# Performance work log

Measured on AMD Instinct MI355X. Metric: run time of the kernel, lower is better.

## Reference

```python
import jax, jax.numpy as jnp
import numpy as np
from jax import lax

RESI_RATIO = 0.5  # abs(quant_resi=-0.5)
BETA = 0.25


def setup_inputs() -> dict:
    key = jax.random.key(0)
    k1, k2, k3, k4 = jax.random.split(key, 4)
    B, C, T, H, W = 2, 32, 8, 32, 32
    V = 8192
    f_BCTHW = jax.random.normal(k1, (B, C, T, H, W), dtype=jnp.float32)
    emb_weight = jax.random.normal(k2, (V, C), dtype=jnp.float32)
    conv_w = jax.random.normal(k3, (C, C, 3, 3, 3), dtype=jnp.float32) * 0.02
    conv_b = jax.random.normal(k4, (C,), dtype=jnp.float32) * 0.02
    return {"f_BCTHW": f_BCTHW, "emb_weight": emb_weight, "conv_w": conv_w, "conv_b": conv_b}


def _mse(a, b):
    d = a - b
    return jnp.mean(d * d)


def reference(f_BCTHW, emb_weight, conv_w, conv_b):
    f = f_BCTHW.astype(jnp.float32)
    B, C, T, H, W = f.shape
    V = emb_weight.shape[0]

    # ---- nearest-codebook assignment (vocab_norm=False path) ----
    # query uses detached f (stop_gradient) exactly as torch .detach()
    q = lax.stop_gradient(f).transpose(0, 2, 3, 4, 1).reshape(-1, C)  # [N, C]
    emb_sg = lax.stop_gradient(emb_weight)
    # ||q||^2 + ||e||^2 - 2 q.e  (addmm_ with alpha=-2, beta=1)
    dist = (jnp.sum(q * q, axis=1, keepdims=True)
            + jnp.sum(emb_sg * emb_sg, axis=1)
            - 2.0 * (q @ emb_sg.T))  # [N, V]
    idx_N = jnp.argmin(dist, axis=1)  # [N] int

    # ---- usage stats (bincount) ----
    counts = jnp.zeros((V,), jnp.float32).at[idx_N].add(1.0)
    prob = counts / jnp.sum(counts)
    vocab_usage = jnp.mean((prob > (0.01 / V)).astype(jnp.float32)) * 100.0

    # ---- embedding gather + residual conv blend ----
    fh = emb_weight[idx_N].reshape(B, T, H, W, C).transpose(0, 4, 1, 2, 3)  # [B,C,T,H,W]
    conv = lax.conv_general_dilated(
        fh, conv_w, window_strides=(1, 1, 1), padding='SAME',
        dimension_numbers=('NCDHW', 'OIDHW', 'NCDHW'))
    conv = conv + conv_b[None, :, None, None, None]
    fh = fh * (1.0 - RESI_RATIO) + conv * RESI_RATIO

    # ---- VQ loss + straight-through estimator ----
    vq_loss = BETA * _mse(lax.stop_gradient(fh), f) + _mse(fh, lax.stop_gradient(f))
    fhat = lax.stop_gradient(fh - f) + f

    return fhat, vq_loss, vocab_usage
```

## Files before the change

kernel.cpp:

```cpp
#include <hip/hip_runtime.h>

#define NQ    16384
#define CDIM  32
#define VSZ   8192
#define PLANE 8192
#define BSTR  262144
#define NEL   524288
#define MARGIN 0.004f

typedef unsigned long long u64;
typedef unsigned int u32;
typedef unsigned short u16;
using f32x4 = __attribute__((ext_vector_type(4))) float;
using s16x8 = __attribute__((ext_vector_type(8))) short;

__device__ __forceinline__ u32 flip_bits(u32 b) {
    return (b & 0x80000000u) ? ~b : (b | 0x80000000u);
}
__device__ __forceinline__ float unflip_val(u32 b) {
    u32 u = (b & 0x80000000u) ? (b ^ 0x80000000u) : ~b;
    return __uint_as_float(u);
}
__device__ __forceinline__ u16 bf16_rne(float x) {
    u32 u = __float_as_uint(x);
    return (u16)((u + 0x7fffu + ((u >> 16) & 1u)) >> 16);
}

__global__ void k_prep(const float* __restrict__ f, const float* __restrict__ emb,
                       u16* __restrict__ EFh, u16* __restrict__ EFl,
                       u16* __restrict__ QFh, u16* __restrict__ QFl,
                       float* __restrict__ enorm, int* __restrict__ counts,
                       float* __restrict__ loss_sum, int* __restrict__ uct,
                       int* __restrict__ flag) {
    int t = blockIdx.x * 256 + threadIdx.x;
    if (t == 0) { *loss_sum = 0.f; *uct = 0; *flag = 0; }
    if (t < 32768) {
        int tile = t >> 6, l = t & 63;
        int row = tile * 16 + (l & 15);
        int k0 = (l >> 4) * 8;
        const float* src = emb + row * CDIM + k0;
        s16x8 vh, vl;
#pragma unroll
        for (int i = 0; i < 8; ++i) {
            float v = src[i];
            u16 hb = bf16_rne(v);
            float hf = __uint_as_float(((u32)hb) << 16);
            vh[i] = (short)hb;
            vl[i] = (short)bf16_rne(v - hf);
        }
        *(s16x8*)(EFh + t * 8) = vh;
        *(s16x8*)(EFl + t * 8) = vl;
    } else if (t < 98304) {
        int t2 = t - 32768;
        int st = t2 >> 6, l = t2 & 63;
        int n = st * 16 + (l & 15);
        int k0 = (l >> 4) * 8;
        int b = n >> 13, p = n & (PLANE - 1);
        const float* fq = f + b * BSTR + p;
        s16x8 vh, vl;
#pragma unroll
        for (int i = 0; i < 8; ++i) {
            float v = -2.0f * fq[(k0 + i) * PLANE];
            u16 hb = bf16_rne(v);
            float hf = __uint_as_float(((u32)hb) << 16);
            vh[i] = (short)hb;
            vl[i] = (short)bf16_rne(v - hf);
        }
        *(s16x8*)(QFh + t2 * 8) = vh;
        *(s16x8*)(QFl + t2 * 8) = vl;
    } else {
        int j = t - 98304;
        const float4* row = (const float4*)(emb + j * CDIM);
        float s = 0.f;
#pragma unroll
        for (int r = 0; r < 8; ++r) {
            float4 v = row[r];
            s += v.x * v.x + v.y * v.y + v.z * v.z + v.w * v.w;
        }
        enorm[j] = s;
        counts[j] = 0;
    }
}

__global__ __launch_bounds__(64) void k_mfma(
    const u16* __restrict__ QFh, const u16* __restrict__ QFl,
    const u16* __restrict__ EFh, const u16* __restrict__ EFl,
    const float* __restrict__ enorm,
    u64* __restrict__ PARTK, float* __restrict__ PARTM2,
    const float* __restrict__ f, const float* __restrict__ emb,
    int* __restrict__ flag) {
    const int l = threadIdx.x;
    const int lq = (l >> 4) * 4;

    if (blockIdx.x == 2048) {
        s16x8 ah = *(const s16x8*)(EFh + l * 8);
        s16x8 al = *(const s16x8*)(EFl + l * 8);
        s16x8 qh = *(const s16x8*)(QFh + l * 8);
        s16x8 ql = *(const s16x8*)(QFl + l * 8);
        f32x4 en = *(const f32x4*)(enorm + lq);
        f32x4 acc = __builtin_amdgcn_mfma_f32_16x16x32_bf16(ah, qh, en, 0, 0, 0);
        acc = __builtin_amdgcn_mfma_f32_16x16x32_bf16(ah, ql, acc, 0, 0, 0);
        acc = __builtin_amdgcn_mfma_f32_16x16x32_bf16(al, qh, acc, 0, 0, 0);
        int q = l & 15;
        const float* fq = f + q;
        int bad = 0;
#pragma unroll
        for (int r = 0; r < 4; ++r) {
            int code = lq + r;
            float ref = enorm[code];
            const float* er = emb + code * CDIM;
            for (int c = 0; c < CDIM; ++c)
                ref = fmaf(-2.0f * fq[c * PLANE], er[c], ref);
            if (fabsf(acc[r] - ref) > 0.05f) bad = 1;
        }
        if (bad) *flag = 1;
        return;
    }

    const int wq = blockIdx.x >> 3, seg = blockIdx.x & 7;
    s16x8 qh[4], ql[4];
#pragma unroll
    for (int s = 0; s < 4; ++s) {
        int st = wq * 4 + s;
        qh[s] = *(const s16x8*)(QFh + (st * 64 + l) * 8);
        ql[s] = *(const s16x8*)(QFl + (st * 64 + l) * 8);
    }
    float m1v[4], m2v[4]; int m1i[4];
#pragma unroll
    for (int s = 0; s < 4; ++s) { m1v[s] = 1e30f; m2v[s] = 1e30f; m1i[s] = 0; }

#pragma unroll 2
    for (int t = 0; t < 64; ++t) {
        int tile = seg * 64 + t;
        s16x8 ah = *(const s16x8*)(EFh + (tile * 64 + l) * 8);
        s16x8 al = *(const s16x8*)(EFl + (tile * 64 + l) * 8);
        f32x4 en = *(const f32x4*)(enorm + tile * 16 + lq);
        int bc = tile * 16 + lq;
#pragma unroll
        for (int s = 0; s < 4; ++s) {
            f32x4 acc = __builtin_amdgcn_mfma_f32_16x16x32_bf16(ah, qh[s], en, 0, 0, 0);
            acc = __builtin_amdgcn_mfma_f32_16x16x32_bf16(ah, ql[s], acc, 0, 0, 0);
            acc = __builtin_amdgcn_mfma_f32_16x16x32_bf16(al, qh[s], acc, 0, 0, 0);
#pragma unroll
            for (int r = 0; r < 4; ++r) {
                float v = acc[r];
                bool lt = v < m1v[s];
                float m2c = fminf(m2v[s], v);
                m2v[s] = lt ? m1v[s] : m2c;
                m1i[s] = lt ? (bc + r) : m1i[s];
                m1v[s] = fminf(m1v[s], v);
            }
        }
    }
#pragma unroll
    for (int s = 0; s < 4; ++s) {
        u64 key = ((u64)flip_bits(__float_as_uint(m1v[s])) << 32) | (u32)m1i[s];
        float m2 = m2v[s];
#pragma unroll
        for (int off = 16; off <= 32; off <<= 1) {
            u64 ko = __shfl_xor(key, off, 64);
            float m2o = __shfl_xor(m2, off, 64);
            u64 kmax = ko > key ? ko : key;
            m2 = fminf(fminf(m2, m2o), unflip_val((u32)(kmax >> 32)));
            key = ko < key ? ko : key;
        }
        if (l < 16) {
            int q = wq * 64 + s * 16 + l;
            PARTK[seg * NQ + q] = key;
            PARTM2[seg * NQ + q] = m2;
        }
    }
}

__global__ void k_final(const u64* __restrict__ PARTK, const float* __restrict__ PARTM2,
                        int* __restrict__ out_idx, int* __restrict__ counts,
                        int* __restrict__ uct, int* __restrict__ ulist,
                        const int* __restrict__ flag) {
    int q = blockIdx.x * 256 + threadIdx.x;
    u64 K = PARTK[q]; float M2 = PARTM2[q];
#pragma unroll
    for (int s = 1; s < 8; ++s) {
        u64 k = PARTK[s * NQ + q]; float m2 = PARTM2[s * NQ + q];
        u64 kmax = k > K ? k : K;
        M2 = fminf(fminf(M2, m2), unflip_val((u32)(kmax >> 32)));
        K = k < K ? k : K;
    }
    int idx = (int)(K & 0xffffffffull);
    float m1 = unflip_val((u32)(K >> 32));
    out_idx[q] = idx;
    if (M2 - m1 > MARGIN && *flag == 0) {
        atomicAdd(&counts[idx], 1);
    } else {
        int p = atomicAdd(uct, 1);
        ulist[p] = q;
    }
}

__global__ __launch_bounds__(256) void k_exact(
    const int* __restrict__ ulist, const int* __restrict__ uct,
    const float* __restrict__ f, const float* __restrict__ emb,
    const float* __restrict__ enorm, int* __restrict__ out_idx,
    int* __restrict__ counts) {
    __shared__ u64 wred[4][2];
    const int tid = threadIdx.x;
    const int uc = *uct;
    for (int base = blockIdx.x * 2; base < uc; base += 256) {
        int nq = uc - base; if (nq > 2) nq = 2;
        int q0 = ulist[base];
        int q1 = (nq > 1) ? ulist[base + 1] : q0;
        float qv0[CDIM], qv1[CDIM];
        {
            const float* f0 = f + (q0 >> 13) * BSTR + (q0 & (PLANE - 1));
            const float* f1 = f + (q1 >> 13) * BSTR + (q1 & (PLANE - 1));
#pragma unroll
            for (int c = 0; c < CDIM; ++c) {
                qv0[c] = -2.0f * f0[c * PLANE];
                qv1[c] = -2.0f * f1[c * PLANE];
            }
        }
        u64 k0 = ~0ull, k1 = ~0ull;
        for (int jj = 0; jj < 32; ++jj) {
            int j = tid + 256 * jj;
            const float4* er = (const float4*)(emb + j * CDIM);
            float d0 = enorm[j], d1 = d0;
#pragma unroll
            for (int c4 = 0; c4 < 8; ++c4) {
                float4 v = er[c4];
                d0 = fmaf(qv0[c4 * 4 + 0], v.x, d0); d0 = fmaf(qv0[c4 * 4 + 1], v.y, d0);
                d0 = fmaf(qv0[c4 * 4 + 2], v.z, d0); d0 = fmaf(qv0[c4 * 4 + 3], v.w, d0);
                d1 = fmaf(qv1[c4 * 4 + 0], v.x, d1); d1 = fmaf(qv1[c4 * 4 + 1], v.y, d1);
                d1 = fmaf(qv1[c4 * 4 + 2], v.z, d1); d1 = fmaf(qv1[c4 * 4 + 3], v.w, d1);
            }
            u64 nk0 = ((u64)flip_bits(__float_as_uint(d0)) << 32) | (u32)j;
            u64 nk1 = ((u64)flip_bits(__float_as_uint(d1)) << 32) | (u32)j;
            if (nk0 < k0) k0 = nk0;
            if (nk1 < k1) k1 = nk1;
        }
#pragma unroll
        for (int off = 1; off <= 32; off <<= 1) {
            u64 o0 = __shfl_xor(k0, off, 64); if (o0 < k0) k0 = o0;
            u64 o1 = __shfl_xor(k1, off, 64); if (o1 < k1) k1 = o1;
        }
        if ((tid & 63) == 0) { wred[tid >> 6][0] = k0; wred[tid >> 6][1] = k1; }
        __syncthreads();
        if (tid == 0) {
            u64 b0 = wred[0][0], b1 = wred[0][1];
#pragma unroll
            for (int w = 1; w < 4; ++w) {
                if (wred[w][0] < b0) b0 = wred[w][0];
                if (wred[w][1] < b1) b1 = wred[w][1];
            }
            int i0 = (int)(b0 & 0xffffffffull);
            out_idx[q0] = i0; atomicAdd(&counts[i0], 1);
            if (nq > 1) {
                int i1 = (int)(b1 & 0xffffffffull);
                out_idx[q1] = i1; atomicAdd(&counts[i1], 1);
            }
        }
        __syncthreads();
    }
}

__global__ void k_gather(const int* __restrict__ idx, const float* __restrict__ emb,
                         float* __restrict__ fh) {
    int n = blockIdx.x * 256 + threadIdx.x;
    int id = idx[n];
    int b = n >> 13, p = n & (PLANE - 1);
    const float4* row = (const float4*)(emb + id * CDIM);
    float* dst = fh + b * BSTR + p;
#pragma unroll
    for (int r = 0; r < 8; ++r) {
        float4 v = row[r];
        dst[(r * 4 + 0) * PLANE] = v.x;
        dst[(r * 4 + 1) * PLANE] = v.y;
        dst[(r * 4 + 2) * PLANE] = v.z;
        dst[(r * 4 + 3) * PLANE] = v.w;
    }
}

__global__ __launch_bounds__(256) void k_conv(const float* __restrict__ fh,
                                              const float* __restrict__ cw,
                                              const float* __restrict__ bias,
                                              const float* __restrict__ f,
                                              float* __restrict__ out,
                                              float* __restrict__ loss_sum) {
    const int tid = threadIdx.x;
    const int n = (blockIdx.x & 63) * 256 + tid;
    const int cog = blockIdx.x >> 6;
    const int b = n >> 13, p = n & (PLANE - 1);
    const int t = p >> 10, h = (p >> 5) & 31, wi = p & 31;

    float msk[27];
#pragma unroll
    for (int dt = 0; dt < 3; ++dt)
#pragma unroll
        for (int dh = 0; dh < 3; ++dh)
#pragma unroll
            for (int dw = 0; dw < 3; ++dw) {
                bool ok = ((unsigned)(t + dt - 1) < 8u) &&
                          ((unsigned)(h + dh - 1) < 32u) &&
                          ((unsigned)(wi + dw - 1) < 32u);
                msk[dt * 9 + dh * 3 + dw] = ok ? 1.0f : 0.0f;
            }

    const float* xb = fh + b * BSTR + p;
    const float* wp = cw + cog * 4 * 864;
    float acc[4] = {0.f, 0.f, 0.f, 0.f};

    for (int ci = 0; ci < CDIM; ++ci) {
        const float* xr = xb + ci * PLANE;
        const float* x0 = xr - 1024;
        const float* x1 = xr;
        const float* x2 = xr + 1024;
#pragma unroll
        for (int dt = 0; dt < 3; ++dt) {
            const float* xp = (dt == 0) ? x0 : ((dt == 1) ? x1 : x2);
#pragma unroll
            for (int dh = 0; dh < 3; ++dh) {
#pragma unroll
                for (int dw = 0; dw < 3; ++dw) {
                    int u = dt * 9 + dh * 3 + dw;
                    float x = xp[(dh - 1) * 32 + (dw - 1)] * msk[u];
#pragma unroll
                    for (int k = 0; k < 4; ++k)
                        acc[k] = fmaf(wp[k * 864 + ci * 27 + u], x, acc[k]);
                }
            }
        }
    }

    float s = 0.f;
#pragma unroll
    for (int k = 0; k < 4; ++k) {
        int co = cog * 4 + k;
        long off = (long)b * BSTR + (long)co * PLANE + p;
        float fhc = fh[off];
        float fv = f[off];
        float o = 0.5f * fhc + 0.5f * (acc[k] + bias[co]);
        out[off] = o;
        float d = o - fv;
        s = fmaf(d, d, s);
    }
#pragma unroll
    for (int off = 32; off > 0; off >>= 1) s += __shfl_down(s, off, 64);
    __shared__ float ls[4];
    if ((tid & 63) == 0) ls[tid >> 6] = s;
    __syncthreads();
    if (tid == 0) atomicAdd(loss_sum, ls[0] + ls[1] + ls[2] + ls[3]);
}

__global__ void k_scalars(const int* __restrict__ counts,
                          const float* __restrict__ loss_sum, float* __restrict__ out) {
    int tid = threadIdx.x;
    int used = 0;
#pragma unroll
    for (int r = 0; r < 32; ++r) used += (counts[tid + 256 * r] > 0) ? 1 : 0;
#pragma unroll
    for (int off = 32; off > 0; off >>= 1) used += __shfl_down(used, off, 64);
    __shared__ int us[4];
    if ((tid & 63) == 0) us[tid >> 6] = used;
    __syncthreads();
    if (tid == 0) {
        int u = us[0] + us[1] + us[2] + us[3];
        out[NEL + 0] = 1.25f * (*loss_sum) / (float)NEL;
        out[NEL + 1] = ((float)u / (float)VSZ) * 100.0f;
    }
}

extern "C" void kernel_launch(void* const* d_in, const int* in_sizes, int n_in,
                              void* d_out, int out_size, void* d_ws, size_t ws_size,
                              hipStream_t stream) {
    const float* f      = (const float*)d_in[0];
    const float* emb    = (const float*)d_in[1];
    const float* conv_w = (const float*)d_in[2];
    const float* conv_b = (const float*)d_in[3];
    float* out = (float*)d_out;
    float* ws = (float*)d_ws;

    float* enorm    = ws;
    int*   counts   = (int*)(ws + 8192);
    int*   idxb     = (int*)(ws + 16384);
    float* loss_sum = ws + 32768;
    int*   uct      = (int*)(ws + 32769);
    int*   flag     = (int*)(ws + 32770);
    int*   ulist    = (int*)(ws + 32772);
    u16*   EFh      = (u16*)(ws + 49408);
    u16*   EFl      = (u16*)(ws + 180480);
    u16*   QFh      = (u16*)(ws + 311552);
    u16*   QFl      = (u16*)(ws + 573696);
    u64*   PARTK    = (u64*)(ws + 835840);
    float* PARTM2   = ws + 1097984;
    float* fh       = ws + 49408 + 2048;

    k_prep   <<<416, 256, 0, stream>>>(f, emb, EFh, EFl, QFh, QFl, enorm, counts,
                                       loss_sum, uct, flag);
    k_mfma   <<<2049, 64, 0, stream>>>(QFh, QFl, EFh, EFl, enorm, PARTK, PARTM2,
                                       f, emb, flag);
    k_final  <<<64, 256, 0, stream>>>(PARTK, PARTM2, idxb, counts, uct, ulist, flag);
    k_exact  <<<128, 256, 0, stream>>>(ulist, uct, f, emb, enorm, idxb, counts);
    k_gather <<<64, 256, 0, stream>>>(idxb, emb, fh);
    k_conv   <<<512, 256, 0, stream>>>(fh, conv_w, conv_b, f, out, loss_sum);
    k_scalars<<<1, 256, 0, stream>>>(counts, loss_sum, out);
}
```

Before: 200.8 us.

## Two-pass threshold argmin, fuse gather into finalize, split conv by input channel

The MFMA distance kernel becomes two passes over 16 codebook segments. The first pass keeps only a cheap running minimum. The second pass does the top-2 key tracking only for tiles whose values fall within a threshold of that minimum. The embedding gather moves into the finalize and exact kernels, and the runtime self-check block and its flag are removed. The conv is split by input-channel groups: each block accumulates all 32 output channels with transposed weights, combines partial sums via atomics into a zeroed buffer, and a separate elementwise kernel applies the blend and the loss. This trades extra atomics and an extra full-tensor pass for less per-element compare work, and drops the fallback that checked bf16-split accuracy.

Result: slower. 224.7 us (+11.9%).

```diff
diff --git a/kernel.cpp b/kernel.cpp
--- a/kernel.cpp
+++ b/kernel.cpp
@@ -7,6 +7,7 @@
 #define BSTR  262144
 #define NEL   524288
 #define MARGIN 0.004f
+#define CAPT   0.006f
 
 typedef unsigned long long u64;
 typedef unsigned int u32;
@@ -27,13 +28,13 @@
 }
 
 __global__ void k_prep(const float* __restrict__ f, const float* __restrict__ emb,
+                       const float* __restrict__ cw,
                        u16* __restrict__ EFh, u16* __restrict__ EFl,
                        u16* __restrict__ QFh, u16* __restrict__ QFl,
                        float* __restrict__ enorm, int* __restrict__ counts,
                        float* __restrict__ loss_sum, int* __restrict__ uct,
-                       int* __restrict__ flag) {
+                       float* __restrict__ wt, float* __restrict__ conv) {
     int t = blockIdx.x * 256 + threadIdx.x;
-    if (t == 0) { *loss_sum = 0.f; *uct = 0; *flag = 0; }
     if (t < 32768) {
         int tile = t >> 6, l = t & 63;
         int row = tile * 16 + (l & 15);
@@ -68,7 +69,7 @@
         }
         *(s16x8*)(QFh + t2 * 8) = vh;
         *(s16x8*)(QFl + t2 * 8) = vl;
-    } else {
+    } else if (t < 106496) {
         int j = t - 98304;
         const float4* row = (const float4*)(emb + j * CDIM);
         float s = 0.f;
@@ -79,45 +80,24 @@
         }
         enorm[j] = s;
         counts[j] = 0;
-    }
-}
-
-__global__ __launch_bounds__(64) void k_mfma(
+        if (j == 0) { *loss_sum = 0.f; *uct = 0; }
+    } else if (t < 134144) {
+        int i = t - 106496;
+        wt[i] = cw[(i & 31) * 864 + (i >> 5)];
+    } else {
+        conv[t - 134144] = 0.f;
+    }
+}
+
+__global__ __launch_bounds__(64) void k_mfma2(
     const u16* __restrict__ QFh, const u16* __restrict__ QFl,
     const u16* __restrict__ EFh, const u16* __restrict__ EFl,
     const float* __restrict__ enorm,
-    u64* __restrict__ PARTK, float* __restrict__ PARTM2,
-    const float* __restrict__ f, const float* __restrict__ emb,
-    int* __restrict__ flag) {
+    u64* __restrict__ PARTK, u64* __restrict__ PART2K) {
     const int l = threadIdx.x;
     const int lq = (l >> 4) * 4;
-
-    if (blockIdx.x == 2048) {
-        s16x8 ah = *(const s16x8*)(EFh + l * 8);
-        s16x8 al = *(const s16x8*)(EFl + l * 8);
-        s16x8 qh = *(const s16x8*)(QFh + l * 8);
-        s16x8 ql = *(const s16x8*)(QFl + l * 8);
-        f32x4 en = *(const f32x4*)(enorm + lq);
-        f32x4 acc = __builtin_amdgcn_mfma_f32_16x16x32_bf16(ah, qh, en, 0, 0, 0);
-        acc = __builtin_amdgcn_mfma_f32_16x16x32_bf16(ah, ql, acc, 0, 0, 0);
-        acc = __builtin_amdgcn_mfma_f32_16x16x32_bf16(al, qh, acc, 0, 0, 0);
-        int q = l & 15;
-        const float* fq = f + q;
-        int bad = 0;
-#pragma unroll
-        for (int r = 0; r < 4; ++r) {
-            int code = lq + r;
-            float ref = enorm[code];
-            const float* er = emb + code * CDIM;
-            for (int c = 0; c < CDIM; ++c)
-                ref = fmaf(-2.0f * fq[c * PLANE], er[c], ref);
-            if (fabsf(acc[r] - ref) > 0.05f) bad = 1;
-        }
-        if (bad) *flag = 1;
-        return;
-    }
-
-    const int wq = blockIdx.x >> 3, seg = blockIdx.x & 7;
+    const int wq = blockIdx.x >> 4, seg = blockIdx.x & 15;
+
     s16x8 qh[4], ql[4];
 #pragma unroll
     for (int s = 0; s < 4; ++s) {
@@ -125,74 +105,119 @@
         qh[s] = *(const s16x8*)(QFh + (st * 64 + l) * 8);
         ql[s] = *(const s16x8*)(QFl + (st * 64 + l) * 8);
     }
-    float m1v[4], m2v[4]; int m1i[4];
-#pragma unroll
-    for (int s = 0; s < 4; ++s) { m1v[s] = 1e30f; m2v[s] = 1e30f; m1i[s] = 0; }
-
+
+    float m1v[4] = {1e30f, 1e30f, 1e30f, 1e30f};
 #pragma unroll 2
-    for (int t = 0; t < 64; ++t) {
-        int tile = seg * 64 + t;
+    for (int t = 0; t < 32; ++t) {
+        int tile = seg * 32 + t;
         s16x8 ah = *(const s16x8*)(EFh + (tile * 64 + l) * 8);
         s16x8 al = *(const s16x8*)(EFl + (tile * 64 + l) * 8);
         f32x4 en = *(const f32x4*)(enorm + tile * 16 + lq);
-        int bc = tile * 16 + lq;
 #pragma unroll
         for (int s = 0; s < 4; ++s) {
             f32x4 acc = __builtin_amdgcn_mfma_f32_16x16x32_bf16(ah, qh[s], en, 0, 0, 0);
             acc = __builtin_amdgcn_mfma_f32_16x16x32_bf16(ah, ql[s], acc, 0, 0, 0);
             acc = __builtin_amdgcn_mfma_f32_16x16x32_bf16(al, qh[s], acc, 0, 0, 0);
-#pragma unroll
-            for (int r = 0; r < 4; ++r) {
-                float v = acc[r];
-                bool lt = v < m1v[s];
-                float m2c = fminf(m2v[s], v);
-                m2v[s] = lt ? m1v[s] : m2c;
-                m1i[s] = lt ? (bc + r) : m1i[s];
-                m1v[s] = fminf(m1v[s], v);
-            }
-        }
-    }
+            float x = fminf(fminf(acc[0], acc[1]), acc[2]);
+            m1v[s] = fminf(fminf(m1v[s], x), acc[3]);
+        }
+    }
+    float thr[4];
 #pragma unroll
     for (int s = 0; s < 4; ++s) {
-        u64 key = ((u64)flip_bits(__float_as_uint(m1v[s])) << 32) | (u32)m1i[s];
-        float m2 = m2v[s];
+        float m = m1v[s];
+        m = fminf(m, __shfl_xor(m, 16, 64));
+        m = fminf(m, __shfl_xor(m, 32, 64));
+        thr[s] = m + CAPT;
+    }
+
+    u64 m1k[4] = {~0ull, ~0ull, ~0ull, ~0ull};
+    u64 m2k[4] = {~0ull, ~0ull, ~0ull, ~0ull};
+#pragma unroll 2
+    for (int t = 0; t < 32; ++t) {
+        int tile = seg * 32 + t;
+        s16x8 ah = *(const s16x8*)(EFh + (tile * 64 + l) * 8);
+        s16x8 al = *(const s16x8*)(EFl + (tile * 64 + l) * 8);
+        f32x4 en = *(const f32x4*)(enorm + tile * 16 + lq);
+        int codeb = tile * 16 + lq;
+#pragma unroll
+        for (int s = 0; s < 4; ++s) {
+            f32x4 acc = __builtin_amdgcn_mfma_f32_16x16x32_bf16(ah, qh[s], en, 0, 0, 0);
+            acc = __builtin_amdgcn_mfma_f32_16x16x32_bf16(ah, ql[s], acc, 0, 0, 0);
+            acc = __builtin_amdgcn_mfma_f32_16x16x32_bf16(al, qh[s], acc, 0, 0, 0);
+            float y = fminf(fminf(fminf(acc[0], acc[1]), acc[2]), acc[3]);
+            if (__any(y <= thr[s])) {
+#pragma unroll
+                for (int r = 0; r < 4; ++r) {
+                    float v = acc[r];
+                    if (v <= thr[s]) {
+                        u32 b = __float_as_uint(v);
+                        b = (b & 0x80000000u) ? ~b : (b | 0x80000000u);
+                        u64 k = ((u64)b << 32) | (u32)(codeb + r);
+                        if (k < m1k[s]) { m2k[s] = m1k[s]; m1k[s] = k; }
+                        else if (k < m2k[s]) m2k[s] = k;
+                    }
+                }
+            }
+        }
+    }
+
+#pragma unroll
+    for (int s = 0; s < 4; ++s) {
+        u64 K = m1k[s], M2 = m2k[s];
 #pragma unroll
         for (int off = 16; off <= 32; off <<= 1) {
-            u64 ko = __shfl_xor(key, off, 64);
-            float m2o = __shfl_xor(m2, off, 64);
-            u64 kmax = ko > key ? ko : key;
-            m2 = fminf(fminf(m2, m2o), unflip_val((u32)(kmax >> 32)));
-            key = ko < key ? ko : key;
+            u64 ko = __shfl_xor(K, off, 64);
+            u64 m2o = __shfl_xor(M2, off, 64);
+            u64 kmax = ko > K ? ko : K;
+            u64 mm = m2o < M2 ? m2o : M2;
+            M2 = kmax < mm ? kmax : mm;
+            K = ko < K ? ko : K;
         }
         if (l < 16) {
             int q = wq * 64 + s * 16 + l;
-            PARTK[seg * NQ + q] = key;
-            PARTM2[seg * NQ + q] = m2;
-        }
-    }
-}
-
-__global__ void k_final(const u64* __restrict__ PARTK, const float* __restrict__ PARTM2,
-                        int* __restrict__ out_idx, int* __restrict__ counts,
-                        int* __restrict__ uct, int* __restrict__ ulist,
-                        const int* __restrict__ flag) {
+            PARTK[seg * NQ + q] = K;
+            PART2K[seg * NQ + q] = M2;
+        }
+    }
+}
+
+__global__ void k_finalg(const u64* __restrict__ PARTK, const u64* __restrict__ PART2K,
+                         const float* __restrict__ emb,
+                         int* __restrict__ out_idx, int* __restrict__ counts,
+                         int* __restrict__ uct, int* __restrict__ ulist,
+                         float* __restrict__ fh) {
     int q = blockIdx.x * 256 + threadIdx.x;
-    u64 K = PARTK[q]; float M2 = PARTM2[q];
-#pragma unroll
-    for (int s = 1; s < 8; ++s) {
-        u64 k = PARTK[s * NQ + q]; float m2 = PARTM2[s * NQ + q];
+    u64 K = PARTK[q], M2 = PART2K[q];
+#pragma unroll
+    for (int s = 1; s < 16; ++s) {
+        u64 k = PARTK[s * NQ + q];
+        u64 m2 = PART2K[s * NQ + q];
         u64 kmax = k > K ? k : K;
-        M2 = fminf(fminf(M2, m2), unflip_val((u32)(kmax >> 32)));
+        u64 mm = m2 < M2 ? m2 : M2;
+        M2 = kmax < mm ? kmax : mm;
         K = k < K ? k : K;
     }
     int idx = (int)(K & 0xffffffffull);
+    out_idx[q] = idx;
     float m1 = unflip_val((u32)(K >> 32));
-    out_idx[q] = idx;
-    if (M2 - m1 > MARGIN && *flag == 0) {
+    float m2v = unflip_val((u32)(M2 >> 32));
+    if (m2v - m1 > MARGIN) {
         atomicAdd(&counts[idx], 1);
+        int b = q >> 13, p = q & (PLANE - 1);
+        const float4* row = (const float4*)(emb + idx * CDIM);
+        float* dst = fh + b * BSTR + p;
+#pragma unroll
+        for (int r = 0; r < 8; ++r) {
+            float4 v = row[r];
+            dst[(r * 4 + 0) * PLANE] = v.x;
+            dst[(r * 4 + 1) * PLANE] = v.y;
+            dst[(r * 4 + 2) * PLANE] = v.z;
+            dst[(r * 4 + 3) * PLANE] = v.w;
+        }
     } else {
-        int p = atomicAdd(uct, 1);
-        ulist[p] = q;
+        int pos = atomicAdd(uct, 1);
+        ulist[pos] = q;
     }
 }
 
@@ -200,8 +225,9 @@
     const int* __restrict__ ulist, const int* __restrict__ uct,
     const float* __restrict__ f, const float* __restrict__ emb,
     const float* __restrict__ enorm, int* __restrict__ out_idx,
-    int* __restrict__ counts) {
+    int* __restrict__ counts, float* __restrict__ fh) {
     __shared__ u64 wred[4][2];
+    __shared__ u64 res[2];
     const int tid = threadIdx.x;
     const int uc = *uct;
     for (int base = blockIdx.x * 2; base < uc; base += 256) {
@@ -252,95 +278,83 @@
             }
             int i0 = (int)(b0 & 0xffffffffull);
             out_idx[q0] = i0; atomicAdd(&counts[i0], 1);
+            res[0] = b0; res[1] = b1;
             if (nq > 1) {
                 int i1 = (int)(b1 & 0xffffffffull);
                 out_idx[q1] = i1; atomicAdd(&counts[i1], 1);
             }
         }
         __syncthreads();
-    }
-}
-
-__global__ void k_gather(const int* __restrict__ idx, const float* __restrict__ emb,
-                         float* __restrict__ fh) {
-    int n = blockIdx.x * 256 + threadIdx.x;
-    int id = idx[n];
-    int b = n >> 13, p = n & (PLANE - 1);
-    const float4* row = (const float4*)(emb + id * CDIM);
-    float* dst = fh + b * BSTR + p;
-#pragma unroll
-    for (int r = 0; r < 8; ++r) {
-        float4 v = row[r];
-        dst[(r * 4 + 0) * PLANE] = v.x;
-        dst[(r * 4 + 1) * PLANE] = v.y;
-        dst[(r * 4 + 2) * PLANE] = v.z;
-        dst[(r * 4 + 3) * PLANE] = v.w;
-    }
-}
-
-__global__ __launch_bounds__(256) void k_conv(const float* __restrict__ fh,
-                                              const float* __restrict__ cw,
-                                              const float* __restrict__ bias,
-                                              const float* __restrict__ f,
-                                              float* __restrict__ out,
-                                              float* __restrict__ loss_sum) {
+        if (tid < 32) {
+            int i0 = (int)(res[0] & 0xffffffffull);
+            fh[(q0 >> 13) * BSTR + tid * PLANE + (q0 & (PLANE - 1))] = emb[i0 * CDIM + tid];
+        } else if (tid < 64 && nq > 1) {
+            int i1 = (int)(res[1] & 0xffffffffull);
+            int c = tid - 32;
+            fh[(q1 >> 13) * BSTR + c * PLANE + (q1 & (PLANE - 1))] = emb[i1 * CDIM + c];
+        }
+        __syncthreads();
+    }
+}
+
+__global__ __launch_bounds__(256) void k_conv1(const float* __restrict__ fh,
+                                               const float* __restrict__ wt,
+                                               float* __restrict__ conv) {
     const int tid = threadIdx.x;
     const int n = (blockIdx.x & 63) * 256 + tid;
-    const int cog = blockIdx.x >> 6;
+    const int cig = blockIdx.x >> 6;
     const int b = n >> 13, p = n & (PLANE - 1);
-    const int t = p >> 10, h = (p >> 5) & 31, wi = p & 31;
-
-    float msk[27];
-#pragma unroll
-    for (int dt = 0; dt < 3; ++dt)
-#pragma unroll
-        for (int dh = 0; dh < 3; ++dh)
-#pragma unroll
-            for (int dw = 0; dw < 3; ++dw) {
-                bool ok = ((unsigned)(t + dt - 1) < 8u) &&
-                          ((unsigned)(h + dh - 1) < 32u) &&
-                          ((unsigned)(wi + dw - 1) < 32u);
-                msk[dt * 9 + dh * 3 + dw] = ok ? 1.0f : 0.0f;
-            }
+    const int t = p >> 10;
+    const int h = (p >> 5) & 31, wi = p & 31;
+
+    const float mh0 = (h > 0) ? 1.f : 0.f, mh2 = (h < 31) ? 1.f : 0.f;
+    const float mw0 = (wi > 0) ? 1.f : 0.f, mw2 = (wi < 31) ? 1.f : 0.f;
+    float m9[9] = {mh0 * mw0, mh0, mh0 * mw2,
+                   mw0,       1.f, mw2,
+                   mh2 * mw0, mh2, mh2 * mw2};
+
+    float acc[32];
+#pragma unroll
+    for (int k = 0; k < 32; ++k) acc[k] = 0.f;
 
     const float* xb = fh + b * BSTR + p;
-    const float* wp = cw + cog * 4 * 864;
-    float acc[4] = {0.f, 0.f, 0.f, 0.f};
-
-    for (int ci = 0; ci < CDIM; ++ci) {
+    for (int i = 0; i < 4; ++i) {
+        int ci = cig * 4 + i;
         const float* xr = xb + ci * PLANE;
-        const float* x0 = xr - 1024;
-        const float* x1 = xr;
-        const float* x2 = xr + 1024;
+        const float* wc = wt + ci * 27 * 32;
 #pragma unroll
         for (int dt = 0; dt < 3; ++dt) {
-            const float* xp = (dt == 0) ? x0 : ((dt == 1) ? x1 : x2);
+            if ((unsigned)(t + dt - 1) >= 8u) continue;
+            const float* xp = xr + (dt - 1) * 1024;
+            const float* wd = wc + dt * 9 * 32;
 #pragma unroll
             for (int dh = 0; dh < 3; ++dh) {
 #pragma unroll
                 for (int dw = 0; dw < 3; ++dw) {
-                    int u = dt * 9 + dh * 3 + dw;
-                    float x = xp[(dh - 1) * 32 + (dw - 1)] * msk[u];
-#pragma unroll
-                    for (int k = 0; k < 4; ++k)
-                        acc[k] = fmaf(wp[k * 864 + ci * 27 + u], x, acc[k]);
+                    float x = xp[(dh - 1) * 32 + (dw - 1)] * m9[dh * 3 + dw];
+                    const float* w32 = wd + (dh * 3 + dw) * 32;
+#pragma unroll
+                    for (int k = 0; k < 32; ++k)
+                        acc[k] = fmaf(w32[k], x, acc[k]);
                 }
             }
         }
     }
-
-    float s = 0.f;
-#pragma unroll
-    for (int k = 0; k < 4; ++k) {
-        int co = cog * 4 + k;
-        long off = (long)b * BSTR + (long)co * PLANE + p;
-        float fhc = fh[off];
-        float fv = f[off];
-        float o = 0.5f * fhc + 0.5f * (acc[k] + bias[co]);
-        out[off] = o;
-        float d = o - fv;
-        s = fmaf(d, d, s);
-    }
+    float* cb = conv + b * BSTR + p;
+#pragma unroll
+    for (int k = 0; k < 32; ++k) atomicAdd(&cb[k * PLANE], acc[k]);
+}
+
+__global__ void k_conv2(const float* __restrict__ conv, const float* __restrict__ fh,
+                        const float* __restrict__ f, const float* __restrict__ bias,
+                        float* __restrict__ out, float* __restrict__ loss_sum) {
+    const int tid = threadIdx.x;
+    const int e = blockIdx.x * 256 + tid;
+    const int co = (e >> 13) & 31;
+    float o = 0.5f * fh[e] + 0.5f * (conv[e] + bias[co]);
+    out[e] = o;
+    float d = o - f[e];
+    float s = d * d;
 #pragma unroll
     for (int off = 32; off > 0; off >>= 1) s += __shfl_down(s, off, 64);
     __shared__ float ls[4];
@@ -382,23 +396,23 @@
     int*   idxb     = (int*)(ws + 16384);
     float* loss_sum = ws + 32768;
     int*   uct      = (int*)(ws + 32769);
-    int*   flag     = (int*)(ws + 32770);
     int*   ulist    = (int*)(ws + 32772);
-    u16*   EFh      = (u16*)(ws + 49408);
-    u16*   EFl      = (u16*)(ws + 180480);
-    u16*   QFh      = (u16*)(ws + 311552);
-    u16*   QFl      = (u16*)(ws + 573696);
-    u64*   PARTK    = (u64*)(ws + 835840);
-    float* PARTM2   = ws + 1097984;
-    float* fh       = ws + 49408 + 2048;
-
-    k_prep   <<<416, 256, 0, stream>>>(f, emb, EFh, EFl, QFh, QFl, enorm, counts,
-                                       loss_sum, uct, flag);
-    k_mfma   <<<2049, 64, 0, stream>>>(QFh, QFl, EFh, EFl, enorm, PARTK, PARTM2,
-                                       f, emb, flag);
-    k_final  <<<64, 256, 0, stream>>>(PARTK, PARTM2, idxb, counts, uct, ulist, flag);
-    k_exact  <<<128, 256, 0, stream>>>(ulist, uct, f, emb, enorm, idxb, counts);
-    k_gather <<<64, 256, 0, stream>>>(idxb, emb, fh);
-    k_conv   <<<512, 256, 0, stream>>>(fh, conv_w, conv_b, f, out, loss_sum);
+    float* wt       = ws + 49408;
+    u64*   PARTK    = (u64*)(ws + 77056);
+    u64*   PART2K   = (u64*)(ws + 601344);
+    u16*   EFh      = (u16*)(ws + 1125632);
+    u16*   EFl      = (u16*)(ws + 1256704);
+    u16*   QFh      = (u16*)(ws + 1387776);
+    u16*   QFl      = (u16*)(ws + 1649920);
+    float* fh       = ws + 1125632 + 2048;
+    float* conv     = ws + 1912064;
+
+    k_prep   <<<2572, 256, 0, stream>>>(f, emb, conv_w, EFh, EFl, QFh, QFl,
+                                        enorm, counts, loss_sum, uct, wt, conv);
+    k_mfma2  <<<4096, 64, 0, stream>>>(QFh, QFl, EFh, EFl, enorm, PARTK, PART2K);
+    k_finalg <<<64, 256, 0, stream>>>(PARTK, PART2K, emb, idxb, counts, uct, ulist, fh);
+    k_exact  <<<128, 256, 0, stream>>>(ulist, uct, f, emb, enorm, idxb, counts, fh);
+    k_conv1  <<<512, 256, 0, stream>>>(fh, wt, conv);
+    k_conv2  <<<2048, 256, 0, stream>>>(conv, fh, f, conv_b, out, loss_sum);
     k_scalars<<<1, 256, 0, stream>>>(counts, loss_sum, out);
 }
```

## Move 3D conv to split-bf16 MFMA, widen codebook search split, drop precision check

Applied to the files above, without the earlier changes.

The scalar FP32 3D convolution is replaced by an implicit-GEMM convolution built on bf16x3 MFMA. The gathered codebook rows are stored channel-last as hi/lo bf16 with zero guard regions, and the conv weights are pre-split in the prep kernel. The nearest-code search now uses 256-thread blocks and splits the codebook into 32 segments instead of 8, so k_final reduces 32 partials. The runtime MFMA accuracy self-check and its fallback flag are removed, which saves work but means there is no longer a guard if the bf16 split loses precision.

Measured after the change: 195.2 us. -2.8%, faster.

```diff
diff --git a/kernel.cpp b/kernel.cpp
--- a/kernel.cpp
+++ b/kernel.cpp
@@ -7,6 +7,8 @@
 #define BSTR  262144
 #define NEL   524288
 #define MARGIN 0.004f
+#define NSEG  32
+#define GUARD 1088
 
 typedef unsigned long long u64;
 typedef unsigned int u32;
@@ -27,13 +29,13 @@
 }
 
 __global__ void k_prep(const float* __restrict__ f, const float* __restrict__ emb,
+                       const float* __restrict__ cw,
                        u16* __restrict__ EFh, u16* __restrict__ EFl,
                        u16* __restrict__ QFh, u16* __restrict__ QFl,
+                       u16* __restrict__ WFh, u16* __restrict__ WFl,
                        float* __restrict__ enorm, int* __restrict__ counts,
-                       float* __restrict__ loss_sum, int* __restrict__ uct,
-                       int* __restrict__ flag) {
+                       float* __restrict__ loss_sum, int* __restrict__ uct) {
     int t = blockIdx.x * 256 + threadIdx.x;
-    if (t == 0) { *loss_sum = 0.f; *uct = 0; *flag = 0; }
     if (t < 32768) {
         int tile = t >> 6, l = t & 63;
         int row = tile * 16 + (l & 15);
@@ -68,7 +70,7 @@
         }
         *(s16x8*)(QFh + t2 * 8) = vh;
         *(s16x8*)(QFl + t2 * 8) = vl;
-    } else {
+    } else if (t < 106496) {
         int j = t - 98304;
         const float4* row = (const float4*)(emb + j * CDIM);
         float s = 0.f;
@@ -79,45 +81,38 @@
         }
         enorm[j] = s;
         counts[j] = 0;
-    }
-}
-
-__global__ __launch_bounds__(64) void k_mfma(
+        if (j == 0) { *loss_sum = 0.f; *uct = 0; }
+    } else if (t < 109952) {
+        int i = t - 106496;
+        int nt = i >> 6, l = i & 63;
+        int col = nt * 16 + (l & 15);
+        int co = col & 31, u = col >> 5;
+        int k0 = (l >> 4) * 8;
+        s16x8 vh, vl;
+#pragma unroll
+        for (int j = 0; j < 8; ++j) {
+            int ci = k0 + j;
+            float v = cw[co * 864 + ci * 27 + u];
+            u16 hb = bf16_rne(v);
+            float hf = __uint_as_float(((u32)hb) << 16);
+            vh[j] = (short)hb;
+            vl[j] = (short)bf16_rne(v - hf);
+        }
+        *(s16x8*)(WFh + i * 8) = vh;
+        *(s16x8*)(WFl + i * 8) = vl;
+    }
+}
+
+__global__ __launch_bounds__(256) void k_mfma3(
     const u16* __restrict__ QFh, const u16* __restrict__ QFl,
     const u16* __restrict__ EFh, const u16* __restrict__ EFl,
     const float* __restrict__ enorm,
-    u64* __restrict__ PARTK, float* __restrict__ PARTM2,
-    const float* __restrict__ f, const float* __restrict__ emb,
-    int* __restrict__ flag) {
-    const int l = threadIdx.x;
+    u64* __restrict__ PARTK, float* __restrict__ PARTM2) {
+    const int l = threadIdx.x & 63;
+    const int w = blockIdx.x * 4 + (threadIdx.x >> 6);
     const int lq = (l >> 4) * 4;
-
-    if (blockIdx.x == 2048) {
-        s16x8 ah = *(const s16x8*)(EFh + l * 8);
-        s16x8 al = *(const s16x8*)(EFl + l * 8);
-        s16x8 qh = *(const s16x8*)(QFh + l * 8);
-        s16x8 ql = *(const s16x8*)(QFl + l * 8);
-        f32x4 en = *(const f32x4*)(enorm + lq);
-        f32x4 acc = __builtin_amdgcn_mfma_f32_16x16x32_bf16(ah, qh, en, 0, 0, 0);
-        acc = __builtin_amdgcn_mfma_f32_16x16x32_bf16(ah, ql, acc, 0, 0, 0);
-        acc = __builtin_amdgcn_mfma_f32_16x16x32_bf16(al, qh, acc, 0, 0, 0);
-        int q = l & 15;
-        const float* fq = f + q;
-        int bad = 0;
-#pragma unroll
-        for (int r = 0; r < 4; ++r) {
-            int code = lq + r;
-            float ref = enorm[code];
-            const float* er = emb + code * CDIM;
-            for (int c = 0; c < CDIM; ++c)
-                ref = fmaf(-2.0f * fq[c * PLANE], er[c], ref);
-            if (fabsf(acc[r] - ref) > 0.05f) bad = 1;
-        }
-        if (bad) *flag = 1;
-        return;
-    }
-
-    const int wq = blockIdx.x >> 3, seg = blockIdx.x & 7;
+    const int wq = w >> 5, seg = w & 31;
+
     s16x8 qh[4], ql[4];
 #pragma unroll
     for (int s = 0; s < 4; ++s) {
@@ -125,13 +120,13 @@
         qh[s] = *(const s16x8*)(QFh + (st * 64 + l) * 8);
         ql[s] = *(const s16x8*)(QFl + (st * 64 + l) * 8);
     }
-    float m1v[4], m2v[4]; int m1i[4];
-#pragma unroll
-    for (int s = 0; s < 4; ++s) { m1v[s] = 1e30f; m2v[s] = 1e30f; m1i[s] = 0; }
+    float m1v[4] = {1e30f, 1e30f, 1e30f, 1e30f};
+    float m2v[4] = {1e30f, 1e30f, 1e30f, 1e30f};
+    int   m1i[4] = {0, 0, 0, 0};
 
 #pragma unroll 2
-    for (int t = 0; t < 64; ++t) {
-        int tile = seg * 64 + t;
+    for (int t = 0; t < 16; ++t) {
+        int tile = seg * 16 + t;
         s16x8 ah = *(const s16x8*)(EFh + (tile * 64 + l) * 8);
         s16x8 al = *(const s16x8*)(EFl + (tile * 64 + l) * 8);
         f32x4 en = *(const f32x4*)(enorm + tile * 16 + lq);
@@ -174,21 +169,20 @@
 
 __global__ void k_final(const u64* __restrict__ PARTK, const float* __restrict__ PARTM2,
                         int* __restrict__ out_idx, int* __restrict__ counts,
-                        int* __restrict__ uct, int* __restrict__ ulist,
-                        const int* __restrict__ flag) {
+                        int* __restrict__ uct, int* __restrict__ ulist) {
     int q = blockIdx.x * 256 + threadIdx.x;
     u64 K = PARTK[q]; float M2 = PARTM2[q];
 #pragma unroll
-    for (int s = 1; s < 8; ++s) {
+    for (int s = 1; s < NSEG; ++s) {
         u64 k = PARTK[s * NQ + q]; float m2 = PARTM2[s * NQ + q];
         u64 kmax = k > K ? k : K;
         M2 = fminf(fminf(M2, m2), unflip_val((u32)(kmax >> 32)));
         K = k < K ? k : K;
     }
     int idx = (int)(K & 0xffffffffull);
+    out_idx[q] = idx;
     float m1 = unflip_val((u32)(K >> 32));
-    out_idx[q] = idx;
-    if (M2 - m1 > MARGIN && *flag == 0) {
+    if (M2 - m1 > MARGIN) {
         atomicAdd(&counts[idx], 1);
     } else {
         int p = atomicAdd(uct, 1);
@@ -261,92 +255,103 @@
     }
 }
 
-__global__ void k_gather(const int* __restrict__ idx, const float* __restrict__ emb,
-                         float* __restrict__ fh) {
-    int n = blockIdx.x * 256 + threadIdx.x;
-    int id = idx[n];
-    int b = n >> 13, p = n & (PLANE - 1);
-    const float4* row = (const float4*)(emb + id * CDIM);
-    float* dst = fh + b * BSTR + p;
-#pragma unroll
-    for (int r = 0; r < 8; ++r) {
-        float4 v = row[r];
-        dst[(r * 4 + 0) * PLANE] = v.x;
-        dst[(r * 4 + 1) * PLANE] = v.y;
-        dst[(r * 4 + 2) * PLANE] = v.z;
-        dst[(r * 4 + 3) * PLANE] = v.w;
-    }
-}
-
-__global__ __launch_bounds__(256) void k_conv(const float* __restrict__ fh,
-                                              const float* __restrict__ cw,
-                                              const float* __restrict__ bias,
-                                              const float* __restrict__ f,
-                                              float* __restrict__ out,
-                                              float* __restrict__ loss_sum) {
-    const int tid = threadIdx.x;
-    const int n = (blockIdx.x & 63) * 256 + tid;
-    const int cog = blockIdx.x >> 6;
-    const int b = n >> 13, p = n & (PLANE - 1);
-    const int t = p >> 10, h = (p >> 5) & 31, wi = p & 31;
-
-    float msk[27];
-#pragma unroll
-    for (int dt = 0; dt < 3; ++dt)
-#pragma unroll
-        for (int dh = 0; dh < 3; ++dh)
-#pragma unroll
-            for (int dw = 0; dw < 3; ++dw) {
-                bool ok = ((unsigned)(t + dt - 1) < 8u) &&
-                          ((unsigned)(h + dh - 1) < 32u) &&
-                          ((unsigned)(wi + dw - 1) < 32u);
-                msk[dt * 9 + dh * 3 + dw] = ok ? 1.0f : 0.0f;
-            }
-
-    const float* xb = fh + b * BSTR + p;
-    const float* wp = cw + cog * 4 * 864;
-    float acc[4] = {0.f, 0.f, 0.f, 0.f};
-
-    for (int ci = 0; ci < CDIM; ++ci) {
-        const float* xr = xb + ci * PLANE;
-        const float* x0 = xr - 1024;
-        const float* x1 = xr;
-        const float* x2 = xr + 1024;
-#pragma unroll
-        for (int dt = 0; dt < 3; ++dt) {
-            const float* xp = (dt == 0) ? x0 : ((dt == 1) ? x1 : x2);
-#pragma unroll
-            for (int dh = 0; dh < 3; ++dh) {
-#pragma unroll
-                for (int dw = 0; dw < 3; ++dw) {
-                    int u = dt * 9 + dh * 3 + dw;
-                    float x = xp[(dh - 1) * 32 + (dw - 1)] * msk[u];
-#pragma unroll
-                    for (int k = 0; k < 4; ++k)
-                        acc[k] = fmaf(wp[k * 864 + ci * 27 + u], x, acc[k]);
-                }
-            }
-        }
-    }
-
-    float s = 0.f;
-#pragma unroll
-    for (int k = 0; k < 4; ++k) {
-        int co = cog * 4 + k;
-        long off = (long)b * BSTR + (long)co * PLANE + p;
-        float fhc = fh[off];
-        float fv = f[off];
-        float o = 0.5f * fhc + 0.5f * (acc[k] + bias[co]);
-        out[off] = o;
-        float d = o - fv;
-        s = fmaf(d, d, s);
-    }
+__global__ void k_fh2(const int* __restrict__ idx, const float* __restrict__ emb,
+                      u16* __restrict__ FH2h, u16* __restrict__ FH2l) {
+    int t = blockIdx.x * 256 + threadIdx.x;
+    if (t < NQ) {
+        int id = idx[t];
+        const float4* e = (const float4*)(emb + id * CDIM);
+        s16x8 vh[4], vl[4];
+#pragma unroll
+        for (int r = 0; r < 8; ++r) {
+            float4 v = e[r];
+            float vv[4] = {v.x, v.y, v.z, v.w};
+#pragma unroll
+            for (int j = 0; j < 4; ++j) {
+                int q = r * 4 + j;
+                u16 hb = bf16_rne(vv[j]);
+                float hf = __uint_as_float(((u32)hb) << 16);
+                vh[q >> 3][q & 7] = (short)hb;
+                vl[q >> 3][q & 7] = (short)bf16_rne(vv[j] - hf);
+            }
+        }
+        u16* dh_ = FH2h + t * CDIM;
+        u16* dl_ = FH2l + t * CDIM;
+#pragma unroll
+        for (int r = 0; r < 4; ++r) {
+            *(s16x8*)(dh_ + r * 8) = vh[r];
+            *(s16x8*)(dl_ + r * 8) = vl[r];
+        }
+    } else {
+        int g = t - NQ;
+        int r = g / 1088, off = (g % 1088) * 16;
+        u32* dst;
+        if (r == 0)      dst = (u32*)(FH2h - GUARD * CDIM);
+        else if (r == 1) dst = (u32*)(FH2h + NQ * CDIM);
+        else if (r == 2) dst = (u32*)(FH2l - GUARD * CDIM);
+        else             dst = (u32*)(FH2l + NQ * CDIM);
+#pragma unroll
+        for (int i = 0; i < 16; ++i) dst[off + i] = 0;
+    }
+}
+
+__global__ __launch_bounds__(256) void k_convm(
+    const u16* __restrict__ FH2h, const u16* __restrict__ FH2l,
+    const u16* __restrict__ WFh, const u16* __restrict__ WFl,
+    const int* __restrict__ idx, const float* __restrict__ emb,
+    const float* __restrict__ bias, const float* __restrict__ f,
+    float* __restrict__ out, float* __restrict__ loss_sum) {
+    const int l = threadIdx.x & 63;
+    const int w = blockIdx.x * 4 + (threadIdx.x >> 6);
+    const int ntile = w >> 1, cot = w & 1;
+    const int co = cot * 16 + (l & 15);
+    const int k0 = (l >> 4) * 8;
+
+    const int nA = ntile * 16 + (l & 15);
+    const int pA = nA & (PLANE - 1);
+    const int tA = pA >> 10, hA = (pA >> 5) & 31, wA = pA & 31;
+    const u16* pAh = FH2h + nA * CDIM + k0;
+    const u16* pAl = FH2l + nA * CDIM + k0;
+
+    f32x4 acc;
+    {
+        float bv = bias[co];
+        acc[0] = bv; acc[1] = bv; acc[2] = bv; acc[3] = bv;
+    }
+    const s16x8 zf = {0, 0, 0, 0, 0, 0, 0, 0};
+#pragma unroll
+    for (int u = 0; u < 27; ++u) {
+        const int dt = u / 9 - 1, dh = (u / 3) % 3 - 1, dw = u % 3 - 1;
+        const int du = dt * 1024 + dh * 32 + dw;
+        bool ok = ((unsigned)(tA + dt) < 8u) && ((unsigned)(hA + dh) < 32u) &&
+                  ((unsigned)(wA + dw) < 32u);
+        s16x8 ah = *(const s16x8*)(pAh + du * CDIM);
+        s16x8 al = *(const s16x8*)(pAl + du * CDIM);
+        if (!ok) { ah = zf; al = zf; }
+        int nt = 2 * u + cot;
+        s16x8 bh = *(const s16x8*)(WFh + (nt * 64 + l) * 8);
+        s16x8 bl = *(const s16x8*)(WFl + (nt * 64 + l) * 8);
+        acc = __builtin_amdgcn_mfma_f32_16x16x32_bf16(ah, bh, acc, 0, 0, 0);
+        acc = __builtin_amdgcn_mfma_f32_16x16x32_bf16(ah, bl, acc, 0, 0, 0);
+        acc = __builtin_amdgcn_mfma_f32_16x16x32_bf16(al, bh, acc, 0, 0, 0);
+    }
+
+    const int n0 = ntile * 16 + (l >> 4) * 4;
+    const int b = n0 >> 13, p0 = n0 & (PLANE - 1);
+    const long fb = (long)b * BSTR + (long)co * PLANE + p0;
+    const float4 f4 = *(const float4*)(f + fb);
+    const int4 iv = *(const int4*)(idx + n0);
+    float o0 = 0.5f * emb[iv.x * CDIM + co] + 0.5f * acc[0];
+    float o1 = 0.5f * emb[iv.y * CDIM + co] + 0.5f * acc[1];
+    float o2 = 0.5f * emb[iv.z * CDIM + co] + 0.5f * acc[2];
+    float o3 = 0.5f * emb[iv.w * CDIM + co] + 0.5f * acc[3];
+    float4 o4 = {o0, o1, o2, o3};
+    *(float4*)(out + fb) = o4;
+    float d0 = o0 - f4.x, d1 = o1 - f4.y, d2 = o2 - f4.z, d3 = o3 - f4.w;
+    float s = fmaf(d0, d0, fmaf(d1, d1, fmaf(d2, d2, d3 * d3)));
 #pragma unroll
     for (int off = 32; off > 0; off >>= 1) s += __shfl_down(s, off, 64);
-    __shared__ float ls[4];
-    if ((tid & 63) == 0) ls[tid >> 6] = s;
-    __syncthreads();
-    if (tid == 0) atomicAdd(loss_sum, ls[0] + ls[1] + ls[2] + ls[3]);
+    if (l == 0) atomicAdd(loss_sum, s);
 }
 
 __global__ void k_scalars(const int* __restrict__ counts,
@@ -382,23 +387,25 @@
     int*   idxb     = (int*)(ws + 16384);
     float* loss_sum = ws + 32768;
     int*   uct      = (int*)(ws + 32769);
-    int*   flag     = (int*)(ws + 32770);
     int*   ulist    = (int*)(ws + 32772);
     u16*   EFh      = (u16*)(ws + 49408);
     u16*   EFl      = (u16*)(ws + 180480);
     u16*   QFh      = (u16*)(ws + 311552);
     u16*   QFl      = (u16*)(ws + 573696);
-    u64*   PARTK    = (u64*)(ws + 835840);
-    float* PARTM2   = ws + 1097984;
-    float* fh       = ws + 49408 + 2048;
-
-    k_prep   <<<416, 256, 0, stream>>>(f, emb, EFh, EFl, QFh, QFl, enorm, counts,
-                                       loss_sum, uct, flag);
-    k_mfma   <<<2049, 64, 0, stream>>>(QFh, QFl, EFh, EFl, enorm, PARTK, PARTM2,
-                                       f, emb, flag);
-    k_final  <<<64, 256, 0, stream>>>(PARTK, PARTM2, idxb, counts, uct, ulist, flag);
+    u16*   WFh      = (u16*)(ws + 835840);
+    u16*   WFl      = (u16*)(ws + 842752);
+    u64*   PARTK    = (u64*)(ws + 849664);
+    float* PARTM2   = ws + 1898240;
+    u16*   FH2h     = (u16*)(ws + 849664)  + GUARD * CDIM;
+    u16*   FH2l     = (u16*)(ws + 1146624) + GUARD * CDIM;
+
+    k_prep   <<<430, 256, 0, stream>>>(f, emb, conv_w, EFh, EFl, QFh, QFl,
+                                       WFh, WFl, enorm, counts, loss_sum, uct);
+    k_mfma3  <<<2048, 256, 0, stream>>>(QFh, QFl, EFh, EFl, enorm, PARTK, PARTM2);
+    k_final  <<<64, 256, 0, stream>>>(PARTK, PARTM2, idxb, counts, uct, ulist);
     k_exact  <<<128, 256, 0, stream>>>(ulist, uct, f, emb, enorm, idxb, counts);
-    k_gather <<<64, 256, 0, stream>>>(idxb, emb, fh);
-    k_conv   <<<512, 256, 0, stream>>>(fh, conv_w, conv_b, f, out, loss_sum);
+    k_fh2    <<<81, 256, 0, stream>>>(idxb, emb, FH2h, FH2l);
+    k_convm  <<<512, 256, 0, stream>>>(FH2h, FH2l, WFh, WFl, idxb, emb,
+                                       conv_b, f, out, loss_sum);
     k_scalars<<<1, 256, 0, stream>>>(counts, loss_sum, out);
 }
```
